# Performance work log

Measured on AMD Instinct MI355X. Metric: run time of the kernel, lower is better.

The kernel has to match this reference:

```python
import jax, jax.numpy as jnp
import numpy as np

ENC_HID = 512
DEC_HID = 1024
ATTN_DIM = 1024
ATTN_IN = ENC_HID * 2 + DEC_HID  # 2048
B, S = 32, 1024


def setup_inputs() -> dict:
    key = jax.random.key(0)
    k1, k2, k3, k4, k5 = jax.random.split(key, 5)
    decoder_hidden = jax.random.normal(k1, (B, DEC_HID), dtype=jnp.float32)
    encoder_outputs = jax.random.normal(k2, (B, S, 2 * ENC_HID), dtype=jnp.float32)
    # nn.Linear(attn_in, attn_dim): weight [attn_dim, attn_in], bias [attn_dim]
    lim = 1.0 / np.sqrt(ATTN_IN)
    W = jax.random.uniform(k3, (ATTN_IN, ATTN_DIM), jnp.float32, -lim, lim)
    b = jax.random.uniform(k4, (ATTN_DIM,), jnp.float32, -lim, lim)
    v = jax.random.uniform(k5, (ATTN_DIM,), jnp.float32, 0.0, 1.0)
    return {"decoder_hidden": decoder_hidden, "encoder_outputs": encoder_outputs,
            "W": W, "b": b, "v": v}


def reference(decoder_hidden, encoder_outputs, W, b, v):
    # Avoid materializing the repeat+concat: split the Linear weight into the
    # decoder-hidden block and the encoder-outputs block. Same math as
    # tanh(Linear(cat([dec_rep, enc], -1))).
    W_dec = W[:DEC_HID]          # [dec_hid, attn_dim]
    W_enc = W[DEC_HID:]          # [2*enc_hid, attn_dim]
    dec_proj = decoder_hidden @ W_dec + b                     # [B, A]
    enc_proj = jnp.einsum('bse,ea->bsa', encoder_outputs, W_enc)  # [B, S, A]
    energy = jnp.tanh(enc_proj + dec_proj[:, None, :])        # [B, S, A]
    attention = jnp.einsum('bsa,a->bs', energy, v)            # [B, S]
    return jax.nn.softmax(attention, axis=1)
```

## Files before the change

### kernel.cpp

```cpp
#include <hip/hip_runtime.h>
#include <stdint.h>

#define ENC2 1024
#define DECH 1024
#define ADIM 1024
#define BB   32
#define SS   1024
#define MTOT (BB*SS)

typedef _Float16 half_t;
typedef __attribute__((ext_vector_type(8))) _Float16 half8;
typedef __attribute__((ext_vector_type(4))) float    f32x4;

__global__ __launch_bounds__(256) void k_wt(const float* __restrict__ W,
                                            half_t* __restrict__ Wt) {
    __shared__ float tile[64][65];
    const int bx = blockIdx.x & 15;
    const int by = blockIdx.x >> 4;
    const int k0 = bx * 64, n0 = by * 64;
    const int t = threadIdx.x;
    #pragma unroll
    for (int i = 0; i < 16; i++) {
        int idx = t + i * 256;
        int r = idx >> 6, c = idx & 63;
        tile[r][c] = W[(size_t)(DECH + k0 + r) * ADIM + n0 + c];
    }
    __syncthreads();
    #pragma unroll
    for (int i = 0; i < 16; i++) {
        int idx = t + i * 256;
        int rn = idx >> 6, ck = idx & 63;
        Wt[(size_t)(n0 + rn) * ENC2 + k0 + ck] = (half_t)tile[ck][rn];
    }
}

__global__ __launch_bounds__(256) void k_decp(const float* __restrict__ dh,
                                              const float* __restrict__ W,
                                              const float* __restrict__ bias,
                                              float* __restrict__ decp) {
    __shared__ float part[2][128];
    const int b  = blockIdx.x >> 3;
    const int a0 = (blockIdx.x & 7) * 128;
    const int t = threadIdx.x;
    const int col = t & 127, kh = t >> 7;
    const float* dhrow = dh + (size_t)b * DECH + kh * 512;
    const float* Wp    = W + (size_t)(kh * 512) * ADIM + a0 + col;
    float s = 0.f;
    for (int kk = 0; kk < 512; kk++)
        s += dhrow[kk] * Wp[(size_t)kk * ADIM];
    part[kh][col] = s;
    __syncthreads();
    if (t < 128)
        decp[(size_t)b * ADIM + a0 + t] = part[0][t] + part[1][t] + bias[a0 + t];
}

#define BM 128
#define BN 256
#define BK 32
#define LDA 40
#define LDB 40

__global__ __launch_bounds__(512) void k_main(const float* __restrict__ enc,
                                              const half_t* __restrict__ Wt,
                                              const float* __restrict__ decp,
                                              const float* __restrict__ v,
                                              float* __restrict__ scores) {
    __shared__ half_t lsA[2][BM][LDA];
    __shared__ half_t lsB[2][BN][LDB];

    const int bid = blockIdx.x;
    const int nb = bid >> 6;
    const int mg = bid & 63;
    const int n0 = nb * BN;
    const int t = threadIdx.x;
    const int w = t >> 6;
    const int L = t & 63;
    const int wm = w & 1, wn = w >> 1;
    const int lane15 = L & 15, quad = L >> 4;
    const int bIdx = mg >> 1;

    const int arow = t >> 2;
    const int akc  = (t & 3) * 8;
    const int brow = t >> 1;
    const int bkc  = (t & 1) * 16;

    const half_t* WtB = Wt + (size_t)(n0 + brow) * ENC2 + bkc;

    float vv[4], dp[4];
    #pragma unroll
    for (int sn = 0; sn < 4; sn++) {
        int ng = n0 + wn * 64 + sn * 16 + lane15;
        vv[sn] = v[ng];
        dp[sn] = decp[(size_t)bIdx * ADIM + ng];
    }

    for (int mc = 0; mc < 4; mc++) {
        const int m0 = mg * 512 + mc * 128;
        const float* Arow = enc + (size_t)(m0 + arow) * ENC2 + akc;

        f32x4 acc[4][4];
        #pragma unroll
        for (int i = 0; i < 4; i++) {
            #pragma unroll
            for (int j = 0; j < 4; j++) acc[i][j] = (f32x4)0.f;
        }

        float4 ra0, ra1; uint4 rb0, rb1;
        auto loadA = [&](int ks) {
            const float* p = Arow + ks * BK;
            ra0 = *(const float4*)p;
            ra1 = *(const float4*)(p + 4);
        };
        auto loadB = [&](int ks) {
            const half_t* p = WtB + ks * BK;
            rb0 = *(const uint4*)p;
            rb1 = *(const uint4*)(p + 8);
        };
        auto writeL = [&](int pb) {
            half8 ha;
            ha[0] = (half_t)ra0.x; ha[1] = (half_t)ra0.y;
            ha[2] = (half_t)ra0.z; ha[3] = (half_t)ra0.w;
            ha[4] = (half_t)ra1.x; ha[5] = (half_t)ra1.y;
            ha[6] = (half_t)ra1.z; ha[7] = (half_t)ra1.w;
            *(half8*)&lsA[pb][arow][akc] = ha;
            *(uint4*)&lsB[pb][brow][bkc]     = rb0;
            *(uint4*)&lsB[pb][brow][bkc + 8] = rb1;
        };

        loadA(0); loadB(0);
        writeL(0);
        loadA(1); loadB(1);
        __syncthreads();

        for (int ks = 0; ks < ENC2 / BK; ks++) {
            const int cur = ks & 1;
            if (ks < ENC2 / BK - 1) {
                writeL(cur ^ 1);
                if (ks < ENC2 / BK - 2) { loadA(ks + 2); loadB(ks + 2); }
            }
            half8 af[4], bf[4];
            #pragma unroll
            for (int sm = 0; sm < 4; sm++)
                af[sm] = *(const half8*)&lsA[cur][wm * 64 + sm * 16 + lane15][quad * 8];
            #pragma unroll
            for (int sn = 0; sn < 4; sn++)
                bf[sn] = *(const half8*)&lsB[cur][wn * 64 + sn * 16 + lane15][quad * 8];
            #pragma unroll
            for (int sm = 0; sm < 4; sm++) {
                #pragma unroll
                for (int sn = 0; sn < 4; sn++)
                    acc[sm][sn] = __builtin_amdgcn_mfma_f32_16x16x32_f16(
                        af[sm], bf[sn], acc[sm][sn], 0, 0, 0);
            }
            __syncthreads();
        }

        #pragma unroll
        for (int sm = 0; sm < 4; sm++) {
            #pragma unroll
            for (int rr = 0; rr < 4; rr++) {
                float s = 0.f;
                #pragma unroll
                for (int sn = 0; sn < 4; sn++) {
                    float x = acc[sm][sn][rr] + dp[sn];
                    float e  = __builtin_amdgcn_exp2f(x * 2.8853900817779268f);
                    float th = 1.f - 2.f * __builtin_amdgcn_rcpf(e + 1.f);
                    s += th * vv[sn];
                }
                s += __shfl_xor(s, 1, 64);
                s += __shfl_xor(s, 2, 64);
                s += __shfl_xor(s, 4, 64);
                s += __shfl_xor(s, 8, 64);
                if (lane15 == 0) {
                    int mlocal = wm * 64 + sm * 16 + quad * 4 + rr;
                    atomicAdd(&scores[(size_t)m0 + mlocal], s);
                }
            }
        }
    }
}

__global__ __launch_bounds__(256) void k_softmax(const float* __restrict__ scores,
                                                 float* __restrict__ out) {
    __shared__ float red[8];
    const int b = blockIdx.x, t = threadIdx.x;
    const float* row = scores + (size_t)b * SS;
    float x[4];
    #pragma unroll
    for (int i = 0; i < 4; i++) x[i] = row[t + i * 256];
    float mx = fmaxf(fmaxf(x[0], x[1]), fmaxf(x[2], x[3]));
    #pragma unroll
    for (int d = 1; d < 64; d <<= 1) mx = fmaxf(mx, __shfl_xor(mx, d, 64));
    if ((t & 63) == 0) red[t >> 6] = mx;
    __syncthreads();
    mx = fmaxf(fmaxf(red[0], red[1]), fmaxf(red[2], red[3]));
    float e[4], s = 0.f;
    #pragma unroll
    for (int i = 0; i < 4; i++) {
        e[i] = __builtin_amdgcn_exp2f((x[i] - mx) * 1.4426950408889634f);
        s += e[i];
    }
    #pragma unroll
    for (int d = 1; d < 64; d <<= 1) s += __shfl_xor(s, d, 64);
    if ((t & 63) == 0) red[4 + (t >> 6)] = s;
    __syncthreads();
    s = red[4] + red[5] + red[6] + red[7];
    float inv = 1.f / s;
    #pragma unroll
    for (int i = 0; i < 4; i++) out[(size_t)b * SS + t + i * 256] = e[i] * inv;
}

extern "C" void kernel_launch(void* const* d_in, const int* in_sizes, int n_in,
                              void* d_out, int out_size, void* d_ws, size_t ws_size,
                              hipStream_t stream) {
    const float* dh   = (const float*)d_in[0];
    const float* enc  = (const float*)d_in[1];
    const float* W    = (const float*)d_in[2];
    const float* bias = (const float*)d_in[3];
    const float* v    = (const float*)d_in[4];
    float* out = (float*)d_out;

    char* ws = (char*)d_ws;
    half_t* Wt    = (half_t*)ws;
    float*  decp  = (float*)(ws + 2u * 1024 * 1024);
    float*  scores = (float*)(ws + 2u * 1024 * 1024 + 128 * 1024);

    k_wt  <<<256, 256, 0, stream>>>(W, Wt);
    k_decp<<<256, 256, 0, stream>>>(dh, W, bias, decp);
    hipMemsetAsync(scores, 0, (size_t)BB * SS * sizeof(float), stream);
    k_main<<<256, 512, 0, stream>>>(enc, Wt, decp, v, scores);
    k_softmax<<<32, 256, 0, stream>>>(scores, out);
}
```

Measured before the change: 324.5 us.

## Pre-tile swizzled weight blocks, DMA B tiles to LDS, regrid main GEMM

```diff
diff --git a/kernel.cpp b/kernel.cpp
--- a/kernel.cpp
+++ b/kernel.cpp
@@ -6,175 +6,185 @@
 #define ADIM 1024
 #define BB   32
 #define SS   1024
-#define MTOT (BB*SS)
 
 typedef _Float16 half_t;
 typedef __attribute__((ext_vector_type(8))) _Float16 half8;
 typedef __attribute__((ext_vector_type(4))) float    f32x4;
 
+__device__ __forceinline__ void dma16(const half_t* g, half_t* l) {
+    __builtin_amdgcn_global_load_lds((const __attribute__((address_space(1))) void*)g,
+                                     (__attribute__((address_space(3))) void*)l,
+                                     16, 0, 0);
+}
+
 __global__ __launch_bounds__(256) void k_wt(const float* __restrict__ W,
-                                            half_t* __restrict__ Wt) {
-    __shared__ float tile[64][65];
-    const int bx = blockIdx.x & 15;
-    const int by = blockIdx.x >> 4;
-    const int k0 = bx * 64, n0 = by * 64;
+                                            half_t* __restrict__ Wt2) {
+    __shared__ float tile[32][257];
+    const int nb = blockIdx.x >> 5;
+    const int ks = blockIdx.x & 31;
     const int t = threadIdx.x;
     #pragma unroll
-    for (int i = 0; i < 16; i++) {
+    for (int i = 0; i < 32; i++) {
         int idx = t + i * 256;
-        int r = idx >> 6, c = idx & 63;
-        tile[r][c] = W[(size_t)(DECH + k0 + r) * ADIM + n0 + c];
-    }
-    __syncthreads();
-    #pragma unroll
-    for (int i = 0; i < 16; i++) {
-        int idx = t + i * 256;
-        int rn = idx >> 6, ck = idx & 63;
-        Wt[(size_t)(n0 + rn) * ENC2 + k0 + ck] = (half_t)tile[ck][rn];
+        int kr = idx >> 8, n = idx & 255;
+        tile[kr][n] = W[(size_t)(DECH + ks * 32 + kr) * ADIM + nb * 256 + n];
+    }
+    __syncthreads();
+    half_t* reg = Wt2 + ((size_t)(nb * 32 + ks) << 13);
+    #pragma unroll
+    for (int i = 0; i < 4; i++) {
+        int cid = t + i * 256;
+        int r = cid >> 2, pos = cid & 3;
+        int c = pos ^ ((r >> 1) & 3);
+        half8 h;
+        #pragma unroll
+        for (int e = 0; e < 8; e++) h[e] = (half_t)tile[c * 8 + e][r];
+        *(half8*)(reg + r * 32 + pos * 8) = h;
     }
 }
 
 __global__ __launch_bounds__(256) void k_decp(const float* __restrict__ dh,
                                               const float* __restrict__ W,
-                                              const float* __restrict__ bias,
                                               float* __restrict__ decp) {
-    __shared__ float part[2][128];
-    const int b  = blockIdx.x >> 3;
-    const int a0 = (blockIdx.x & 7) * 128;
+    const int ct = blockIdx.x & 15;
+    const int kc = blockIdx.x >> 4;
     const int t = threadIdx.x;
-    const int col = t & 127, kh = t >> 7;
-    const float* dhrow = dh + (size_t)b * DECH + kh * 512;
-    const float* Wp    = W + (size_t)(kh * 512) * ADIM + a0 + col;
-    float s = 0.f;
-    for (int kk = 0; kk < 512; kk++)
-        s += dhrow[kk] * Wp[(size_t)kk * ADIM];
-    part[kh][col] = s;
-    __syncthreads();
-    if (t < 128)
-        decp[(size_t)b * ADIM + a0 + t] = part[0][t] + part[1][t] + bias[a0 + t];
+    const int col = ct * 64 + (t & 63);
+    const int wv = __builtin_amdgcn_readfirstlane(t >> 6);
+    const int k0 = kc * 128 + wv * 32;
+    float wreg[32];
+    #pragma unroll
+    for (int kk = 0; kk < 32; kk++)
+        wreg[kk] = W[(size_t)(k0 + kk) * ADIM + col];
+    #pragma unroll 4
+    for (int b = 0; b < 32; b++) {
+        float s = 0.f;
+        #pragma unroll
+        for (int kk = 0; kk < 32; kk++)
+            s += dh[b * 1024 + k0 + kk] * wreg[kk];
+        atomicAdd(&decp[b * 1024 + col], s);
+    }
 }
 
 #define BM 128
 #define BN 256
 #define BK 32
 #define LDA 40
-#define LDB 40
-
-__global__ __launch_bounds__(512) void k_main(const float* __restrict__ enc,
-                                              const half_t* __restrict__ Wt,
-                                              const float* __restrict__ decp,
-                                              const float* __restrict__ v,
-                                              float* __restrict__ scores) {
+
+__global__ __launch_bounds__(512, 6) void k_main(const float* __restrict__ enc,
+                                                 const half_t* __restrict__ Wt2,
+                                                 const float* __restrict__ decp,
+                                                 const float* __restrict__ bias,
+                                                 const float* __restrict__ v,
+                                                 float* __restrict__ scores) {
     __shared__ half_t lsA[2][BM][LDA];
-    __shared__ half_t lsB[2][BN][LDB];
+    __shared__ half_t lsB[2][BN * BK];
 
     const int bid = blockIdx.x;
-    const int nb = bid >> 6;
-    const int mg = bid & 63;
+    const int nb = bid & 3;
+    const int mi = bid >> 2;
+    const int m0 = mi * BM;
     const int n0 = nb * BN;
     const int t = threadIdx.x;
-    const int w = t >> 6;
-    const int L = t & 63;
+    const int w = t >> 6, L = t & 63;
     const int wm = w & 1, wn = w >> 1;
     const int lane15 = L & 15, quad = L >> 4;
-    const int bIdx = mg >> 1;
-
-    const int arow = t >> 2;
-    const int akc  = (t & 3) * 8;
-    const int brow = t >> 1;
-    const int bkc  = (t & 1) * 16;
-
-    const half_t* WtB = Wt + (size_t)(n0 + brow) * ENC2 + bkc;
+    const int batch = mi >> 3;
+
+    const int arow = t & 127;
+    const int akc  = (t >> 7) * 8;
+    const float* Aptr = enc + (size_t)(m0 + arow) * ENC2 + akc;
+
+    const half_t* Bbase = Wt2 + ((size_t)(nb * 32) << 13);
 
     float vv[4], dp[4];
     #pragma unroll
     for (int sn = 0; sn < 4; sn++) {
         int ng = n0 + wn * 64 + sn * 16 + lane15;
         vv[sn] = v[ng];
-        dp[sn] = decp[(size_t)bIdx * ADIM + ng];
-    }
-
-    for (int mc = 0; mc < 4; mc++) {
-        const int m0 = mg * 512 + mc * 128;
-        const float* Arow = enc + (size_t)(m0 + arow) * ENC2 + akc;
-
-        f32x4 acc[4][4];
-        #pragma unroll
-        for (int i = 0; i < 4; i++) {
-            #pragma unroll
-            for (int j = 0; j < 4; j++) acc[i][j] = (f32x4)0.f;
-        }
-
-        float4 ra0, ra1; uint4 rb0, rb1;
-        auto loadA = [&](int ks) {
-            const float* p = Arow + ks * BK;
-            ra0 = *(const float4*)p;
-            ra1 = *(const float4*)(p + 4);
-        };
-        auto loadB = [&](int ks) {
-            const half_t* p = WtB + ks * BK;
-            rb0 = *(const uint4*)p;
-            rb1 = *(const uint4*)(p + 8);
-        };
-        auto writeL = [&](int pb) {
-            half8 ha;
-            ha[0] = (half_t)ra0.x; ha[1] = (half_t)ra0.y;
-            ha[2] = (half_t)ra0.z; ha[3] = (half_t)ra0.w;
-            ha[4] = (half_t)ra1.x; ha[5] = (half_t)ra1.y;
-            ha[6] = (half_t)ra1.z; ha[7] = (half_t)ra1.w;
-            *(half8*)&lsA[pb][arow][akc] = ha;
-            *(uint4*)&lsB[pb][brow][bkc]     = rb0;
-            *(uint4*)&lsB[pb][brow][bkc + 8] = rb1;
-        };
-
-        loadA(0); loadB(0);
-        writeL(0);
-        loadA(1); loadB(1);
-        __syncthreads();
-
-        for (int ks = 0; ks < ENC2 / BK; ks++) {
-            const int cur = ks & 1;
-            if (ks < ENC2 / BK - 1) {
-                writeL(cur ^ 1);
-                if (ks < ENC2 / BK - 2) { loadA(ks + 2); loadB(ks + 2); }
-            }
-            half8 af[4], bf[4];
-            #pragma unroll
-            for (int sm = 0; sm < 4; sm++)
-                af[sm] = *(const half8*)&lsA[cur][wm * 64 + sm * 16 + lane15][quad * 8];
+        dp[sn] = decp[(size_t)batch * ADIM + ng] + bias[ng];
+    }
+
+    f32x4 acc[4][4];
+    #pragma unroll
+    for (int i = 0; i < 4; i++)
+        #pragma unroll
+        for (int j = 0; j < 4; j++) acc[i][j] = (f32x4)0.f;
+
+    float4 ra0, ra1;
+    auto loadA = [&](int ks) {
+        const float* p = Aptr + ks * BK;
+        ra0 = *(const float4*)p;
+        ra1 = *(const float4*)(p + 4);
+    };
+    auto writeA = [&](int pb) {
+        half8 ha;
+        ha[0] = (half_t)ra0.x; ha[1] = (half_t)ra0.y;
+        ha[2] = (half_t)ra0.z; ha[3] = (half_t)ra0.w;
+        ha[4] = (half_t)ra1.x; ha[5] = (half_t)ra1.y;
+        ha[6] = (half_t)ra1.z; ha[7] = (half_t)ra1.w;
+        *(half8*)&lsA[pb][arow][akc] = ha;
+    };
+    auto dmaB = [&](int ks, int pb) {
+        #pragma unroll
+        for (int jj = 0; jj < 2; jj++) {
+            int j = 2 * w + jj;
+            dma16(Bbase + ((size_t)ks << 13) + j * 512 + L * 8,
+                  &lsB[pb][j * 512]);
+        }
+    };
+
+    dmaB(0, 0);
+    loadA(0);
+    writeA(0);
+    loadA(1);
+    __syncthreads();
+
+    for (int ks = 0; ks < ENC2 / BK; ks++) {
+        const int cur = ks & 1;
+        if (ks < ENC2 / BK - 1) {
+            dmaB(ks + 1, cur ^ 1);
+            writeA(cur ^ 1);
+            if (ks < ENC2 / BK - 2) loadA(ks + 2);
+        }
+        half8 af[4], bf[4];
+        #pragma unroll
+        for (int sm = 0; sm < 4; sm++)
+            af[sm] = *(const half8*)&lsA[cur][wm * 64 + sm * 16 + lane15][quad * 8];
+        #pragma unroll
+        for (int sn = 0; sn < 4; sn++) {
+            int r = wn * 64 + sn * 16 + lane15;
+            int pos = quad ^ ((r >> 1) & 3);
+            bf[sn] = *(const half8*)&lsB[cur][r * 32 + pos * 8];
+        }
+        #pragma unroll
+        for (int sm = 0; sm < 4; sm++)
             #pragma unroll
             for (int sn = 0; sn < 4; sn++)
-                bf[sn] = *(const half8*)&lsB[cur][wn * 64 + sn * 16 + lane15][quad * 8];
+                acc[sm][sn] = __builtin_amdgcn_mfma_f32_16x16x32_f16(
+                    af[sm], bf[sn], acc[sm][sn], 0, 0, 0);
+        __syncthreads();
+    }
+
+    #pragma unroll
+    for (int sm = 0; sm < 4; sm++) {
+        #pragma unroll
+        for (int rr = 0; rr < 4; rr++) {
+            float s = 0.f;
             #pragma unroll
-            for (int sm = 0; sm < 4; sm++) {
-                #pragma unroll
-                for (int sn = 0; sn < 4; sn++)
-                    acc[sm][sn] = __builtin_amdgcn_mfma_f32_16x16x32_f16(
-                        af[sm], bf[sn], acc[sm][sn], 0, 0, 0);
+            for (int sn = 0; sn < 4; sn++) {
+                float x = acc[sm][sn][rr] + dp[sn];
+                float e  = __builtin_amdgcn_exp2f(x * 2.8853900817779268f);
+                float th = 1.f - 2.f * __builtin_amdgcn_rcpf(e + 1.f);
+                s += th * vv[sn];
             }
-            __syncthreads();
-        }
-
-        #pragma unroll
-        for (int sm = 0; sm < 4; sm++) {
-            #pragma unroll
-            for (int rr = 0; rr < 4; rr++) {
-                float s = 0.f;
-                #pragma unroll
-                for (int sn = 0; sn < 4; sn++) {
-                    float x = acc[sm][sn][rr] + dp[sn];
-                    float e  = __builtin_amdgcn_exp2f(x * 2.8853900817779268f);
-                    float th = 1.f - 2.f * __builtin_amdgcn_rcpf(e + 1.f);
-                    s += th * vv[sn];
-                }
-                s += __shfl_xor(s, 1, 64);
-                s += __shfl_xor(s, 2, 64);
-                s += __shfl_xor(s, 4, 64);
-                s += __shfl_xor(s, 8, 64);
-                if (lane15 == 0) {
-                    int mlocal = wm * 64 + sm * 16 + quad * 4 + rr;
-                    atomicAdd(&scores[(size_t)m0 + mlocal], s);
-                }
+            s += __shfl_xor(s, 1, 64);
+            s += __shfl_xor(s, 2, 64);
+            s += __shfl_xor(s, 4, 64);
+            s += __shfl_xor(s, 8, 64);
+            if (lane15 == 0) {
+                int mlocal = wm * 64 + sm * 16 + quad * 4 + rr;
+                atomicAdd(&scores[(size_t)m0 + mlocal], s);
             }
         }
     }
@@ -221,13 +231,13 @@
     float* out = (float*)d_out;
 
     char* ws = (char*)d_ws;
-    half_t* Wt    = (half_t*)ws;
+    half_t* Wt2   = (half_t*)ws;
     float*  decp  = (float*)(ws + 2u * 1024 * 1024);
     float*  scores = (float*)(ws + 2u * 1024 * 1024 + 128 * 1024);
 
-    k_wt  <<<256, 256, 0, stream>>>(W, Wt);
-    k_decp<<<256, 256, 0, stream>>>(dh, W, bias, decp);
-    hipMemsetAsync(scores, 0, (size_t)BB * SS * sizeof(float), stream);
-    k_main<<<256, 512, 0, stream>>>(enc, Wt, decp, v, scores);
+    hipMemsetAsync(ws + 2u * 1024 * 1024, 0, 256 * 1024, stream);
+    k_wt  <<<128, 256, 0, stream>>>(W, Wt2);
+    k_decp<<<128, 256, 0, stream>>>(dh, W, decp);
+    k_main<<<1024, 512, 0, stream>>>(enc, Wt2, decp, bias, v, scores);
     k_softmax<<<32, 256, 0, stream>>>(scores, out);
 }
```

Measured after the change: 554.7 us. 70.9% more time.
